# Optimization experiments

Hardware: AMD Instinct MI355X
Metric: run time of the kernel (lower is better)

Reference implementation:

```python
import jax, jax.numpy as jnp
import numpy as np

# FusionTransformer with input_resolution=(1, 8192): window_size collapses to 1,
# shift_size forced to 0, attn_mask is None. Inside WindowAttention each window
# has N=1 token, so the 512-truncation and the stride-2 subsample are no-ops,
# softmax over a single key yields 1, and the attention output equals v.
# We still compute q/k, the scaled logit, the relative-position bias (index
# table is [[0]]) and the softmax faithfully.

B, L, C = 8, 8192, 384
NH, CS = 8, 3
DIN = C // CS              # 128 = dim // channel_scale
HD = C // NH // CS         # 16  = per-head qk/v dim
SCALE = (C // NH) ** -0.5  # uses head_dim = dim // num_heads = 48 (as in source)
HID = int(DIN * 4.0)       # 512 mlp hidden
EPS = 1e-5                 # torch LayerNorm default


def setup_inputs() -> dict:
    key = jax.random.key(0)
    ks = jax.random.split(key, 8)
    w = lambda k, shape: jax.random.normal(k, shape, jnp.float32) * 0.02
    return {
        "x": jax.random.normal(ks[0], (B, L, C), jnp.float32),
        "g1": jnp.ones((C,), jnp.float32), "b1": jnp.zeros((C,), jnp.float32),
        "Wq": w(ks[1], (C, DIN)), "bq": jnp.zeros((DIN,), jnp.float32),
        "Wkv": w(ks[2], (C, 2 * DIN)), "bkv": jnp.zeros((2 * DIN,), jnp.float32),
        "rpb": w(ks[3], (1, NH)),  # (2*ws-1)^2 = 1 table rows at ws=1
        "Wp": w(ks[4], (DIN, DIN)), "bp": jnp.zeros((DIN,), jnp.float32),
        "g2": jnp.ones((DIN,), jnp.float32), "b2": jnp.zeros((DIN,), jnp.float32),
        "W1": w(ks[5], (DIN, HID)), "bm1": jnp.zeros((HID,), jnp.float32),
        "W2": w(ks[6], (HID, DIN)), "bm2": jnp.zeros((DIN,), jnp.float32),
    }


def _ln(x, g, b):
    m = x.mean(-1, keepdims=True)
    v = ((x - m) ** 2).mean(-1, keepdims=True)
    return (x - m) * jax.lax.rsqrt(v + EPS) * g + b


def reference(x, g1, b1, Wq, bq, Wkv, bkv, rpb, Wp, bp, g2, b2, W1, bm1, W2, bm2):
    Bx, Lx, _ = x.shape
    h = _ln(x, g1, b1)                       # norm1
    # window partition with ws=1: every token is a (N=1) window; B_ = B*L.
    q = h @ Wq + bq                          # (B, L, DIN)
    kv = h @ Wkv + bkv                       # (B, L, 2*DIN); split dim-0 of the
    k, v = kv[..., :DIN], kv[..., DIN:]      # reshape(...,2,NH,HD) -> k, v
    qh = q.reshape(Bx, Lx, NH, HD)
    kh = k.reshape(Bx, Lx, NH, HD)
    vh = v.reshape(Bx, Lx, NH, HD)
    # attn logits (B, L, NH, 1, 1) flattened: q*scale . k + rel-pos bias[idx=0]
    logits = jnp.einsum('blhd,blhd->blh', qh * SCALE, kh) + rpb[0]
    attn = jax.nn.softmax(logits[..., None], axis=-1)   # softmax over N=1 keys
    out = (attn * vh).reshape(Bx, Lx, NH * HD)          # attn @ v, heads merged
    y = out @ Wp + bp                                   # proj
    # residual branch: x = attn_out; x = x + mlp(norm2(x))
    z = y + (jax.nn.gelu(_ln(y, g2, b2) @ W1 + bm1, approximate=False) @ W2 + bm2)
    return z
```

## Files before the change

### kernel.cpp

```cpp
#include <hip/hip_runtime.h>
#include <hip/hip_bf16.h>
#include <stdint.h>


typedef __attribute__((ext_vector_type(8))) short bf16x8;
typedef __attribute__((ext_vector_type(4))) float f32x4;

__device__ __forceinline__ short f2bf(float f) {
  union { float f; unsigned u; } a; a.f = f;
  unsigned u = a.u;
  u += 0x7fffu + ((u >> 16) & 1u);
  return (short)(u >> 16);
}
__device__ __forceinline__ float bf2f(short s) {
  union { unsigned u; float f; } a; a.u = ((unsigned)(unsigned short)s) << 16;
  return a.f;
}
__device__ __forceinline__ float gelu_fast(float h) {
  float h2 = h * h;
  float w  = h * (2.3022082f + 0.1029471f * h2);
  float e  = __builtin_amdgcn_exp2f(w);
  float r  = __builtin_amdgcn_rcpf(e + 1.0f);
  return h - h * r;
}
__device__ __forceinline__ void gload_lds16(const void* g, void* l) {
  __builtin_amdgcn_global_load_lds(
      (const __attribute__((address_space(1))) unsigned*)g,
      (__attribute__((address_space(3))) unsigned*)l, 16, 0, 0);
}


__global__ void prep(const float* __restrict__ Wkv, const float* __restrict__ bkv,
                     const float* __restrict__ Wp,  const float* __restrict__ bp,
                     const float* __restrict__ W1,  const float* __restrict__ W2,
                     const float* __restrict__ g1,  const float* __restrict__ b1,
                     const float* __restrict__ g2,  const float* __restrict__ b2,
                     const float* __restrict__ bm1,
                     short* __restrict__ WcT, short* __restrict__ W1Ta,
                     short* __restrict__ W1Tb, short* __restrict__ W2Ta,
                     short* __restrict__ W2Tb, float* __restrict__ bc,
                     float* __restrict__ bm1c) {
  const int b = blockIdx.x, tid = threadIdx.x;
  if (b < 192) {
    __shared__ float wv[2][128];
    const int kk = tid >> 7, n = tid & 127, k = 2 * b + kk;
    wv[kk][n] = Wkv[k * 256 + 128 + n];
    __syncthreads();
    float s0 = 0, s1 = 0, s2 = 0, s3 = 0;
#pragma unroll 8
    for (int m = 0; m < 128; m += 4) {
      s0 += wv[kk][m]     * Wp[(m)     * 128 + n];
      s1 += wv[kk][m + 1] * Wp[(m + 1) * 128 + n];
      s2 += wv[kk][m + 2] * Wp[(m + 2) * 128 + n];
      s3 += wv[kk][m + 3] * Wp[(m + 3) * 128 + n];
    }
    WcT[n * 392 + k] = f2bf(g1[k] * (s0 + s1 + s2 + s3));
  } else if (b == 192) {
    __shared__ float t[128];
    if (tid < 128) {
      float a = 0;
      for (int k = 0; k < 384; ++k) a += b1[k] * Wkv[k * 256 + 128 + tid];
      t[tid] = a + bkv[128 + tid];
    }
    __syncthreads();
    if (tid < 128) {
      float s = bp[tid];
#pragma unroll 8
      for (int m = 0; m < 128; ++m) s += t[m] * Wp[m * 128 + tid];
      bc[tid] = s;
    }
  } else if (b < 449) {
    const int id = (b - 193) * 256 + tid;
    const int n = id & 511, k = id >> 9;
    const short v = f2bf(W1[k * 512 + n] * g2[k]);
    if (n < 256) W1Ta[n * 132 + k] = v;
    else         W1Tb[(n - 256) * 132 + k] = v;
  } else if (b < 705) {
    const int id = (b - 449) * 256 + tid;
    const int n = id & 127, k = id >> 7;
    const int ch = k >> 6, kk = k & 63;
    short* dst = (ch < 4) ? W2Ta : W2Tb;
    dst[((ch & 3) * 128 + n) * 68 + kk] = f2bf(W2[k * 128 + n]);
  } else {
    const int h = (b - 705) * 256 + tid;
    float s = bm1[h];
#pragma unroll 8
    for (int k = 0; k < 128; ++k) s += b2[k] * W1[k * 512 + h];
    bm1c[h] = s;
  }
}

__global__ __launch_bounds__(1024, 4)
void k1(const float* __restrict__ x, const short* __restrict__ WcTg,
        const float* __restrict__ bcg,
        short* __restrict__ yb, short* __restrict__ lb) {
  __shared__ __align__(16) short WcT_l[128 * 392];
  __shared__ float bcf[128];
  const int tid = threadIdx.x, lane = tid & 63, w = tid >> 6;
  const int q = lane >> 4, c16 = lane & 15;

  for (int c = w; c < 98; c += 16)
    gload_lds16((const char*)WcTg + c * 1024 + lane * 16, (char*)WcT_l + c * 1024);
  if (tid < 32) ((float4*)bcf)[tid] = ((const float4*)bcg)[tid];
  __syncthreads();

  float bcv[8];
#pragma unroll
  for (int t = 0; t < 8; ++t) bcv[t] = bcf[t * 16 + c16];

  const long band = (long)blockIdx.x * 16 + w;
  const float* xp = x + (band * 16 + c16) * 384 + q * 8;
  bf16x8 frag[12];
  float s = 0.f, sq = 0.f;
#pragma unroll
  for (int ks = 0; ks < 12; ++ks) {
    const float4 va = *(const float4*)(xp + ks * 32);
    const float4 vb = *(const float4*)(xp + ks * 32 + 4);
    s  += va.x + va.y + va.z + va.w + vb.x + vb.y + vb.z + vb.w;
    sq += va.x * va.x + va.y * va.y + va.z * va.z + va.w * va.w
        + vb.x * vb.x + vb.y * vb.y + vb.z * vb.z + vb.w * vb.w;
    bf16x8 f;
    f[0] = f2bf(va.x); f[1] = f2bf(va.y); f[2] = f2bf(va.z); f[3] = f2bf(va.w);
    f[4] = f2bf(vb.x); f[5] = f2bf(vb.y); f[6] = f2bf(vb.z); f[7] = f2bf(vb.w);
    frag[ks] = f;
  }
  s  += __shfl_xor(s, 16);  s  += __shfl_xor(s, 32);
  sq += __shfl_xor(sq, 16); sq += __shfl_xor(sq, 32);
  const float mean = s * (1.f / 384.f);
  const float rs = rsqrtf(sq * (1.f / 384.f) - mean * mean + 1e-5f);
#pragma unroll
  for (int ks = 0; ks < 12; ++ks) {
    bf16x8 f = frag[ks];
#pragma unroll
    for (int e = 0; e < 8; ++e) f[e] = f2bf((bf2f(f[e]) - mean) * rs);
    frag[ks] = f;
  }
  f32x4 yacc[8];
#pragma unroll
  for (int t = 0; t < 8; ++t) yacc[t] = (f32x4){0.f, 0.f, 0.f, 0.f};
#pragma unroll
  for (int ks = 0; ks < 12; ++ks)
#pragma unroll
    for (int t = 0; t < 8; ++t) {
      bf16x8 bfr = *(const bf16x8*)(WcT_l + (t * 16 + c16) * 392 + ks * 32 + q * 8);
      yacc[t] = __builtin_amdgcn_mfma_f32_16x16x32_bf16(frag[ks], bfr, yacc[t], 0, 0, 0);
    }
  float sm[4] = {0, 0, 0, 0}, sv[4] = {0, 0, 0, 0};
#pragma unroll
  for (int t = 0; t < 8; ++t)
#pragma unroll
    for (int r = 0; r < 4; ++r) {
      yacc[t][r] += bcv[t];
      const float v = yacc[t][r]; sm[r] += v; sv[r] += v * v;
    }
#pragma unroll
  for (int r = 0; r < 4; ++r) {
    sm[r] += __shfl_xor(sm[r], 1); sm[r] += __shfl_xor(sm[r], 2);
    sm[r] += __shfl_xor(sm[r], 4); sm[r] += __shfl_xor(sm[r], 8);
    sv[r] += __shfl_xor(sv[r], 1); sv[r] += __shfl_xor(sv[r], 2);
    sv[r] += __shfl_xor(sv[r], 4); sv[r] += __shfl_xor(sv[r], 8);
  }
  short* ybB = yb + band * 2048;
  short* lbB = lb + band * 2048;
#pragma unroll
  for (int r = 0; r < 4; ++r) {
    const float mn = sm[r] * (1.f / 128.f);
    const float rv = rsqrtf(sv[r] * (1.f / 128.f) - mn * mn + 1e-5f);
    bf16x8 yp;
#pragma unroll
    for (int t = 0; t < 8; ++t) {
      const float yv = yacc[t][r];
      yp[t] = f2bf(yv);
      lbB[((t * 4 + r) * 4 + q) * 16 + c16] = f2bf((yv - mn) * rv);
    }
    *(bf16x8*)(ybB + ((r * 4 + q) * 16 + c16) * 8) = yp;
  }
}

template <bool FINAL>
__global__ __launch_bounds__(1024, 4)
void k2(const short* __restrict__ lb, short* __restrict__ ybuf,
        const short* __restrict__ W1Tg, const short* __restrict__ W2Tg,
        const float* __restrict__ bm1h, const float* __restrict__ bm2,
        float* __restrict__ out) {
  __shared__ __align__(16) short W1s[256 * 132];
  __shared__ __align__(16) short W2s[4 * 128 * 68];
  __shared__ __align__(16) short A3s[16][16 * 36];
  __shared__ float bm1s[256], bm2s[128];
  const int tid = threadIdx.x, lane = tid & 63, w = tid >> 6;
  const int q = lane >> 4, c16 = lane & 15;

  for (int c = w; c < 66; c += 16)
    gload_lds16((const char*)W1Tg + c * 1024 + lane * 16, (char*)W1s + c * 1024);
  for (int c = w; c < 68; c += 16)
    gload_lds16((const char*)W2Tg + c * 1024 + lane * 16, (char*)W2s + c * 1024);
  if (tid < 64) ((float4*)bm1s)[tid] = ((const float4*)bm1h)[tid];
  else if (tid < 96) ((float4*)bm2s)[tid - 64] = ((const float4*)bm2)[tid - 64];
  __syncthreads();

  float bm2v[8];
#pragma unroll
  for (int t = 0; t < 8; ++t) bm2v[t] = bm2s[t * 16 + c16];

  const long band = (long)blockIdx.x * 16 + w;
  const short* lbB = lb + band * 2048;
  short* ybB = ybuf + band * 2048;
  bf16x8 a2f[4];
#pragma unroll
  for (int ks = 0; ks < 4; ++ks) {
    const int t = ks * 2 + (q >> 1);
    a2f[ks] = *(const bf16x8*)(lbB + ((t * 4 + (c16 & 3)) * 4 + (c16 >> 2)) * 16 + (q & 1) * 8);
  }
  f32x4 zacc[8];
#pragma unroll
  for (int t = 0; t < 8; ++t) zacc[t] = (f32x4){0.f, 0.f, 0.f, 0.f};
  short* a3 = A3s[w];

#pragma unroll
  for (int ch = 0; ch < 4; ++ch) {
#pragma unroll
    for (int sub = 0; sub < 2; ++sub) {
      f32x4 hacc[2];
      hacc[0] = (f32x4){0.f, 0.f, 0.f, 0.f};
      hacc[1] = (f32x4){0.f, 0.f, 0.f, 0.f};
#pragma unroll
      for (int ks = 0; ks < 4; ++ks)
#pragma unroll
        for (int tt = 0; tt < 2; ++tt) {
          bf16x8 bfr = *(const bf16x8*)(W1s + (ch * 64 + sub * 32 + tt * 16 + c16) * 132 + ks * 32 + q * 8);
          hacc[tt] = __builtin_amdgcn_mfma_f32_16x16x32_bf16(a2f[ks], bfr, hacc[tt], 0, 0, 0);
        }
#pragma unroll
      for (int tt = 0; tt < 2; ++tt) {
        const float bb = bm1s[ch * 64 + sub * 32 + tt * 16 + c16];
#pragma unroll
        for (int r = 0; r < 4; ++r) {
          const float h = hacc[tt][r] + bb;
          a3[(q * 4 + r) * 36 + tt * 16 + c16] = f2bf(gelu_fast(h));
        }
      }
      asm volatile("s_waitcnt lgkmcnt(0)" ::: "memory");
      bf16x8 af = *(const bf16x8*)(a3 + c16 * 36 + q * 8);
#pragma unroll
      for (int t = 0; t < 8; ++t) {
        bf16x8 bfr = *(const bf16x8*)(W2s + (ch * 128 + t * 16 + c16) * 68 + sub * 32 + q * 8);
        zacc[t] = __builtin_amdgcn_mfma_f32_16x16x32_bf16(af, bfr, zacc[t], 0, 0, 0);
      }
    }
  }
  bf16x8 yf[4];
#pragma unroll
  for (int r = 0; r < 4; ++r)
    yf[r] = *(const bf16x8*)(ybB + ((r * 4 + q) * 16 + c16) * 8);
  if (!FINAL) {
#pragma unroll
    for (int r = 0; r < 4; ++r) {
      bf16x8 zp;
#pragma unroll
      for (int t = 0; t < 8; ++t) zp[t] = f2bf(bf2f(yf[r][t]) + zacc[t][r]);
      *(bf16x8*)(ybB + ((r * 4 + q) * 16 + c16) * 8) = zp;
    }
  } else {
#pragma unroll
    for (int r = 0; r < 4; ++r) {
      const long rowg = band * 16 + q * 4 + r;
#pragma unroll
      for (int t = 0; t < 8; ++t)
        out[rowg * 128 + t * 16 + c16] = bf2f(yf[r][t]) + zacc[t][r] + bm2v[t];
    }
  }
}

extern "C" void kernel_launch(void* const* d_in, const int* in_sizes, int n_in,
                              void* d_out, int out_size, void* d_ws, size_t ws_size,
                              hipStream_t stream) {
  const float* x   = (const float*)d_in[0];
  const float* g1  = (const float*)d_in[1];
  const float* b1  = (const float*)d_in[2];
  const float* Wkv = (const float*)d_in[5];
  const float* bkv = (const float*)d_in[6];
  const float* Wp  = (const float*)d_in[8];
  const float* bp  = (const float*)d_in[9];
  const float* g2  = (const float*)d_in[10];
  const float* b2  = (const float*)d_in[11];
  const float* W1  = (const float*)d_in[12];
  const float* bm1 = (const float*)d_in[13];
  const float* W2  = (const float*)d_in[14];
  const float* bm2 = (const float*)d_in[15];

  char* ws = (char*)d_ws;
  short* WcT  = (short*)(ws + 0);
  short* W1Ta = (short*)(ws + 100352);
  short* W2Ta = (short*)(ws + 167936);
  short* W1Tb = (short*)(ws + 237568);
  short* W2Tb = (short*)(ws + 305152);
  float* bc   = (float*)(ws + 374784);
  float* bm1c = (float*)(ws + 375296);
  short* ybuf = (short*)(ws + 378880);
  short* lb   = (short*)(ws + 17156096);

  prep<<<707, 256, 0, stream>>>(Wkv, bkv, Wp, bp, W1, W2, g1, b1, g2, b2, bm1,
                                WcT, W1Ta, W1Tb, W2Ta, W2Tb, bc, bm1c);
  k1<<<256, 1024, 0, stream>>>(x, WcT, bc, ybuf, lb);
  k2<false><<<256, 1024, 0, stream>>>(lb, ybuf, W1Ta, W2Ta, bm1c, bm2, (float*)d_out);
  k2<true><<<256, 1024, 0, stream>>>(lb, ybuf, W1Tb, W2Tb, bm1c + 256, bm2, (float*)d_out);
}
```

Baseline: 256.0 us.

## Fold LayerNorm normalization into GEMM epilogue via column sums of weights

k1 now feeds raw bf16 x straight into the MFMA instead of normalizing it first. The LayerNorm mean and rstd are applied afterwards using per-output-column sums of the folded weight matrix, computed once per block in shared memory. This drops the second normalization pass over the fragments and lets MFMAs overlap the x loads, at the cost of an extra LDS reduction and barrier per block. It changes numerics slightly because x is rounded before centering. Launch bounds drop the min-blocks hint, and the bias precompute loop is unrolled with four accumulators.

```diff
diff --git a/kernel.cpp b/kernel.cpp
--- a/kernel.cpp
+++ b/kernel.cpp
@@ -58,9 +58,15 @@
   } else if (b == 192) {
     __shared__ float t[128];
     if (tid < 128) {
-      float a = 0;
-      for (int k = 0; k < 384; ++k) a += b1[k] * Wkv[k * 256 + 128 + tid];
-      t[tid] = a + bkv[128 + tid];
+      float a0 = 0, a1 = 0, a2 = 0, a3 = 0;
+#pragma unroll 8
+      for (int k = 0; k < 384; k += 4) {
+        a0 += b1[k]     * Wkv[(k)     * 256 + 128 + tid];
+        a1 += b1[k + 1] * Wkv[(k + 1) * 256 + 128 + tid];
+        a2 += b1[k + 2] * Wkv[(k + 2) * 256 + 128 + tid];
+        a3 += b1[k + 3] * Wkv[(k + 3) * 256 + 128 + tid];
+      }
+      t[tid] = a0 + a1 + a2 + a3 + bkv[128 + tid];
     }
     __syncthreads();
     if (tid < 128) {
@@ -90,12 +96,12 @@
   }
 }
 
-__global__ __launch_bounds__(1024, 4)
+__global__ __launch_bounds__(1024)
 void k1(const float* __restrict__ x, const short* __restrict__ WcTg,
         const float* __restrict__ bcg,
         short* __restrict__ yb, short* __restrict__ lb) {
   __shared__ __align__(16) short WcT_l[128 * 392];
-  __shared__ float bcf[128];
+  __shared__ float bcf[128], css[128];
   const int tid = threadIdx.x, lane = tid & 63, w = tid >> 6;
   const int q = lane >> 4, c16 = lane & 15;
 
@@ -103,14 +109,27 @@
     gload_lds16((const char*)WcTg + c * 1024 + lane * 16, (char*)WcT_l + c * 1024);
   if (tid < 32) ((float4*)bcf)[tid] = ((const float4*)bcg)[tid];
   __syncthreads();
-
-  float bcv[8];
-#pragma unroll
-  for (int t = 0; t < 8; ++t) bcv[t] = bcf[t * 16 + c16];
+  if (tid < 128) {
+    float s0 = 0, s1 = 0, s2 = 0, s3 = 0;
+    const short* row = WcT_l + tid * 392;
+#pragma unroll 12
+    for (int k = 0; k < 384; k += 4) {
+      s0 += bf2f(row[k]); s1 += bf2f(row[k + 1]);
+      s2 += bf2f(row[k + 2]); s3 += bf2f(row[k + 3]);
+    }
+    css[tid] = s0 + s1 + s2 + s3;
+  }
+  __syncthreads();
+
+  float bcv[8], cs[8];
+#pragma unroll
+  for (int t = 0; t < 8; ++t) { bcv[t] = bcf[t * 16 + c16]; cs[t] = css[t * 16 + c16]; }
 
   const long band = (long)blockIdx.x * 16 + w;
   const float* xp = x + (band * 16 + c16) * 384 + q * 8;
-  bf16x8 frag[12];
+  f32x4 yacc[8];
+#pragma unroll
+  for (int t = 0; t < 8; ++t) yacc[t] = (f32x4){0.f, 0.f, 0.f, 0.f};
   float s = 0.f, sq = 0.f;
 #pragma unroll
   for (int ks = 0; ks < 12; ++ks) {
@@ -122,36 +141,29 @@
     bf16x8 f;
     f[0] = f2bf(va.x); f[1] = f2bf(va.y); f[2] = f2bf(va.z); f[3] = f2bf(va.w);
     f[4] = f2bf(vb.x); f[5] = f2bf(vb.y); f[6] = f2bf(vb.z); f[7] = f2bf(vb.w);
-    frag[ks] = f;
+#pragma unroll
+    for (int t = 0; t < 8; ++t) {
+      bf16x8 bfr = *(const bf16x8*)(WcT_l + (t * 16 + c16) * 392 + ks * 32 + q * 8);
+      yacc[t] = __builtin_amdgcn_mfma_f32_16x16x32_bf16(f, bfr, yacc[t], 0, 0, 0);
+    }
   }
   s  += __shfl_xor(s, 16);  s  += __shfl_xor(s, 32);
   sq += __shfl_xor(sq, 16); sq += __shfl_xor(sq, 32);
   const float mean = s * (1.f / 384.f);
   const float rs = rsqrtf(sq * (1.f / 384.f) - mean * mean + 1e-5f);
-#pragma unroll
-  for (int ks = 0; ks < 12; ++ks) {
-    bf16x8 f = frag[ks];
-#pragma unroll
-    for (int e = 0; e < 8; ++e) f[e] = f2bf((bf2f(f[e]) - mean) * rs);
-    frag[ks] = f;
-  }
-  f32x4 yacc[8];
-#pragma unroll
-  for (int t = 0; t < 8; ++t) yacc[t] = (f32x4){0.f, 0.f, 0.f, 0.f};
-#pragma unroll
-  for (int ks = 0; ks < 12; ++ks)
-#pragma unroll
-    for (int t = 0; t < 8; ++t) {
-      bf16x8 bfr = *(const bf16x8*)(WcT_l + (t * 16 + c16) * 392 + ks * 32 + q * 8);
-      yacc[t] = __builtin_amdgcn_mfma_f32_16x16x32_bf16(frag[ks], bfr, yacc[t], 0, 0, 0);
-    }
+  float mr[4], rr[4];
+#pragma unroll
+  for (int r = 0; r < 4; ++r) {
+    mr[r] = __shfl(mean, q * 4 + r);
+    rr[r] = __shfl(rs,   q * 4 + r);
+  }
   float sm[4] = {0, 0, 0, 0}, sv[4] = {0, 0, 0, 0};
 #pragma unroll
   for (int t = 0; t < 8; ++t)
 #pragma unroll
     for (int r = 0; r < 4; ++r) {
-      yacc[t][r] += bcv[t];
-      const float v = yacc[t][r]; sm[r] += v; sv[r] += v * v;
+      const float yv = rr[r] * (yacc[t][r] - mr[r] * cs[t]) + bcv[t];
+      yacc[t][r] = yv; sm[r] += yv; sv[r] += yv * yv;
     }
 #pragma unroll
   for (int r = 0; r < 4; ++r) {
@@ -178,7 +190,7 @@
 }
 
 template <bool FINAL>
-__global__ __launch_bounds__(1024, 4)
+__global__ __launch_bounds__(1024)
 void k2(const short* __restrict__ lb, short* __restrict__ ybuf,
         const short* __restrict__ W1Tg, const short* __restrict__ W2Tg,
         const float* __restrict__ bm1h, const float* __restrict__ bm2,
```

Result: no change. 254.0 us (-0.8%).
